# Optimization experiments

Hardware: AMD Instinct MI355X
Metric: run time of the kernel (lower is better)

## Reference

```python
import jax, jax.numpy as jnp
import numpy as np
from jax import lax

B, C, H, W = 8, 256, 128, 128
O = 256
KH, KW = 1, 3
PH, PW = 0, 1
K = KH * KW


def setup_inputs() -> dict:
    key = jax.random.key(0)
    k1, k2, k3, k4 = jax.random.split(key, 4)
    x = jax.random.normal(k1, (B, C, H, W), jnp.float32)
    # offset-predicting conv (small init so sample points stay near the grid)
    offset_w = jax.random.normal(k2, (2 * K, C, KH, KW), jnp.float32) * 0.01
    offset_b = jax.random.normal(k3, (2 * K,), jnp.float32) * 0.01
    # deformable conv weight, no bias (bias=False in the module)
    deform_w = jax.random.normal(k4, (O, C, KH, KW), jnp.float32) * (1.0 / np.sqrt(C * K))
    return {"x": x, "offset_w": offset_w, "offset_b": offset_b, "deform_w": deform_w}


def _gather_corner(x_flat, yi, xi, valid_dtype):
    # x_flat: [B, C, H*W]; yi, xi: int32 [B, K, Ho, Wo]
    valid = (yi >= 0) & (yi < H) & (xi >= 0) & (xi < W)
    yc = jnp.clip(yi, 0, H - 1)
    xc = jnp.clip(xi, 0, W - 1)
    idx = yc * W + xc  # [B, K, Ho, Wo]
    # per-batch fancy gather -> [B, C, K, Ho, Wo]
    g = jax.vmap(lambda f, i: f[:, i])(x_flat, idx)
    return g * valid[:, None].astype(valid_dtype)


def _deform_conv(x, offset, deform_w):
    # torchvision-style deform_conv2d with zero padding, groups=1, dg=1
    Ho, Wo = offset.shape[2], offset.shape[3]
    off = offset.reshape(B, K, 2, Ho, Wo)
    off_y, off_x = off[:, :, 0], off[:, :, 1]  # [B, K, Ho, Wo]

    k = jnp.arange(K)
    base_y = (-PH + (k // KW)).astype(x.dtype)[None, :, None, None]
    base_x = (-PW + (k % KW)).astype(x.dtype)[None, :, None, None]
    grid_y = jnp.arange(Ho, dtype=x.dtype)[None, None, :, None]
    grid_x = jnp.arange(Wo, dtype=x.dtype)[None, None, None, :]

    py = grid_y + base_y + off_y  # fractional sample rows [B,K,Ho,Wo]
    px = grid_x + base_x + off_x  # fractional sample cols

    y0f = jnp.floor(py)
    x0f = jnp.floor(px)
    wy = (py - y0f)[:, None]  # [B,1,K,Ho,Wo]
    wx = (px - x0f)[:, None]
    y0 = y0f.astype(jnp.int32)
    x0 = x0f.astype(jnp.int32)
    y1 = y0 + 1
    x1 = x0 + 1

    x_flat = x.reshape(B, C, H * W)
    v00 = _gather_corner(x_flat, y0, x0, x.dtype)
    v01 = _gather_corner(x_flat, y0, x1, x.dtype)
    v10 = _gather_corner(x_flat, y1, x0, x.dtype)
    v11 = _gather_corner(x_flat, y1, x1, x.dtype)

    sampled = (v00 * (1 - wy) * (1 - wx) + v01 * (1 - wy) * wx
               + v10 * wy * (1 - wx) + v11 * wy * wx)  # [B,C,K,Ho,Wo]

    return jnp.einsum('bckhw,ock->bohw', sampled, deform_w.reshape(O, C, K))


def reference(x, offset_w, offset_b, deform_w):
    # offset conv (stride 1, padding (0,1))
    offset = lax.conv_general_dilated(x, offset_w, window_strides=(1, 1),
                                      padding=[(PH, PH), (PW, PW)])
    offset = offset + offset_b[None, :, None, None]
    # in-place zeroing from the original forward
    offset = offset.at[:, 1].set(0.0).at[:, 4].set(0.0)
    return _deform_conv(x, offset, deform_w)
```

## Files before the change

kernel.cpp:

```cpp
#include <hip/hip_runtime.h>
#include <hip/hip_bf16.h>
#include <hip/hip_fp16.h>

#define Bn 8
#define Cn 256
#define Hn 128
#define Wn 128
#define On 256
#define HWn (Hn*Wn)
#define Pn  HWn
#define Rpad 896
#define W2ROW 768
#define QC  ((size_t)Pn * Cn)

typedef __attribute__((ext_vector_type(8))) short bf16x8;
typedef __attribute__((ext_vector_type(4))) float f32x4;

__device__ __forceinline__ void gload_lds16(const void* g, void* l) {
  __builtin_amdgcn_global_load_lds(
      (__attribute__((address_space(1))) void*)g,
      (__attribute__((address_space(3))) void*)l, 16, 0, 0);
}

__device__ __forceinline__ unsigned short f2bf(float f) {
  unsigned int u = __float_as_uint(f);
  unsigned int r = (u + 0x7fffu + ((u >> 16) & 1u)) >> 16;
  return (unsigned short)r;
}
__device__ __forceinline__ float bf2f(unsigned short u) {
  return __uint_as_float(((unsigned int)u) << 16);
}
__device__ __forceinline__ float h2f(unsigned int u16) {
  return __half2float(__ushort_as_half((unsigned short)u16));
}
__device__ __forceinline__ void bacc(uint4 v, float w, float* f) {
  f[0] += w * __uint_as_float(v.x << 16);
  f[1] += w * __uint_as_float(v.x & 0xffff0000u);
  f[2] += w * __uint_as_float(v.y << 16);
  f[3] += w * __uint_as_float(v.y & 0xffff0000u);
  f[4] += w * __uint_as_float(v.z << 16);
  f[5] += w * __uint_as_float(v.z & 0xffff0000u);
  f[6] += w * __uint_as_float(v.w << 16);
  f[7] += w * __uint_as_float(v.w & 0xffff0000u);
}

__global__ __launch_bounds__(256) void k_wprep(
    const float* __restrict__ dw, const float* __restrict__ ow,
    unsigned short* __restrict__ W2, unsigned short* __restrict__ Wbig) {
  int r = blockIdx.x;
  int c = threadIdx.x;
  float v = 0.f;
  if (r < 768) {
    int k = r >> 8, o = r & 255;
    v = dw[((size_t)o * Cn + c) * 3 + k];
    W2[(size_t)o * W2ROW + k * 256 + c] = f2bf(v);
  } else if (r < 786) {
    int rr = r - 768;
    int oc = rr / 3, kw = rr - 3 * oc;
    v = ow[((size_t)oc * Cn + c) * 3 + kw];
  }
  Wbig[(size_t)r * Cn + c] = f2bf(v);
}

__global__ __launch_bounds__(256) void k_transpose(
    const float* __restrict__ x, unsigned short* __restrict__ xbT) {
  int b = blockIdx.z;
  int q0 = blockIdx.x * 64, c0 = blockIdx.y * 64;
  __shared__ unsigned short t[64][66];
  int tid = threadIdx.x;
  int qq = (tid & 15) * 4;
  int cb = tid >> 4;
  const float* xb = x + (size_t)b * Cn * HWn;
  #pragma unroll
  for (int i = 0; i < 4; ++i) {
    int cl = cb + 16 * i;
    float4 v = *(const float4*)(xb + (size_t)(c0 + cl) * HWn + q0 + qq);
    unsigned lo = (unsigned)f2bf(v.x) | ((unsigned)f2bf(v.y) << 16);
    unsigned hi = (unsigned)f2bf(v.z) | ((unsigned)f2bf(v.w) << 16);
    *(unsigned*)&t[cl][qq]     = lo;
    *(unsigned*)&t[cl][qq + 2] = hi;
  }
  __syncthreads();
  unsigned short* dst = xbT + (size_t)b * QC;
  int c2 = (tid & 31) * 2, qg = tid >> 5;
  #pragma unroll
  for (int j = 0; j < 8; ++j) {
    int ql = j * 8 + qg;
    unsigned int u = (unsigned int)t[c2][ql] | ((unsigned int)t[c2 + 1][ql] << 16);
    *(unsigned int*)(dst + (size_t)(q0 + ql) * Cn + c0 + c2) = u;
  }
}

__global__ __launch_bounds__(256) void k_goff(
    const unsigned short* __restrict__ xbT,
    const unsigned short* __restrict__ Wbig,
    unsigned short* __restrict__ Goff) {
  int q0 = blockIdx.y * 128;
  const unsigned short* xb = xbT + (size_t)blockIdx.z * QC;
  unsigned short* Gz = Goff + (size_t)blockIdx.z * Pn * 32;
  __shared__ unsigned short Qs[128 * 64];
  __shared__ unsigned short Ws[128 * 64];
  int tid = threadIdx.x;
  int lane = tid & 63, wid = tid >> 6;
  int wr = wid >> 1, wc = wid & 1;
  f32x4 acc[4][4];
  #pragma unroll
  for (int m = 0; m < 4; ++m)
    #pragma unroll
    for (int n = 0; n < 4; ++n) acc[m][n] = (f32x4){0.f, 0.f, 0.f, 0.f};

  for (int kt = 0; kt < 4; ++kt) {
    int ck0 = kt * 64;
    __syncthreads();
    #pragma unroll
    for (int i = 0; i < 4; ++i) {
      int fo = wid * 1024 + i * 4096 + lane * 16;
      int row = fo >> 7;
      int slot = (fo >> 4) & 7;
      int ss = slot ^ (row & 7);
      gload_lds16(xb   + (size_t)(q0 + row) * Cn + ck0 + ss * 8, (char*)Qs + fo);
      gload_lds16(Wbig + (size_t)(768 + row) * Cn + ck0 + ss * 8, (char*)Ws + fo);
    }
    __syncthreads();
    #pragma unroll
    for (int s = 0; s < 2; ++s) {
      bf16x8 af[4], bfr[4];
      #pragma unroll
      for (int m = 0; m < 4; ++m) {
        int row = wr * 64 + m * 16 + (lane & 15);
        int slot = (s * 4 + (lane >> 4)) ^ (row & 7);
        af[m] = *(const bf16x8*)((const char*)Qs + row * 128 + slot * 16);
      }
      #pragma unroll
      for (int n = 0; n < 4; ++n) {
        int row = wc * 64 + n * 16 + (lane & 15);
        int slot = (s * 4 + (lane >> 4)) ^ (row & 7);
        bfr[n] = *(const bf16x8*)((const char*)Ws + row * 128 + slot * 16);
      }
      #pragma unroll
      for (int m = 0; m < 4; ++m)
        #pragma unroll
        for (int n = 0; n < 4; ++n)
          acc[m][n] = __builtin_amdgcn_mfma_f32_16x16x32_bf16(af[m], bfr[n], acc[m][n], 0, 0, 0);
    }
  }
  if (wc == 0) {
    #pragma unroll
    for (int m = 0; m < 4; ++m)
      #pragma unroll
      for (int n = 0; n < 2; ++n)
        #pragma unroll
        for (int rr = 0; rr < 4; ++rr) {
          int q = q0 + wr * 64 + m * 16 + (lane >> 4) * 4 + rr;
          int j = n * 16 + (lane & 15);
          if (j < 18) Gz[(size_t)q * 32 + j] = f2bf(acc[m][n][rr]);
        }
  }
}

__global__ __launch_bounds__(512) void k_fgemm(
    const unsigned short* __restrict__ xbT,
    const unsigned short* __restrict__ W2,
    const unsigned short* __restrict__ Goff,
    const float* __restrict__ obias,
    float* __restrict__ out) {
  int pt = blockIdx.x, z = blockIdx.y;
  int ho = (pt & 7) * 16 + (pt >> 3);
  const unsigned short* xz = xbT + (size_t)z * QC;
  const unsigned short* Gf = Goff + (size_t)z * Pn * 32;

  __shared__ unsigned short Qs[256 * 64];
  __shared__ unsigned short Ss[128 * 64];
  __shared__ unsigned int Sqb[128][3];
  __shared__ unsigned int Swh[128][3][2];

  int tid = threadIdx.x;
  if (tid < 384) {
    int k = tid >> 7;
    int wo = tid & 127;
    float offy = 0.f, offx = 0.f;
    int ocy = 2 * k, ocx = 2 * k + 1;
    if (ocy != 4) {
      float s = obias[ocy];
      #pragma unroll
      for (int kw = 0; kw < 3; ++kw) {
        int col = wo + kw - 1;
        if (col >= 0 && col < Wn)
          s += bf2f(Gf[(size_t)(ho * Wn + col) * 32 + ocy * 3 + kw]);
      }
      offy = s;
    }
    if (ocx != 1) {
      float s = obias[ocx];
      #pragma unroll
      for (int kw = 0; kw < 3; ++kw) {
        int col = wo + kw - 1;
        if (col >= 0 && col < Wn)
          s += bf2f(Gf[(size_t)(ho * Wn + col) * 32 + ocx * 3 + kw]);
      }
      offx = s;
    }
    float py = (float)ho + offy;
    float px = (float)(wo + k - 1) + offx;
    float y0f = floorf(py), x0f = floorf(px);
    float wy = py - y0f, wx = px - x0f;
    int y0 = (int)y0f, x0 = (int)x0f;
    int y1 = y0 + 1, x1 = x0 + 1;
    bool vy0 = (y0 >= 0) && (y0 < Hn), vy1 = (y1 >= 0) && (y1 < Hn);
    bool vx0 = (x0 >= 0) && (x0 < Wn), vx1 = (x1 >= 0) && (x1 < Wn);
    int yc0 = min(max(y0, 0), Hn - 1), yc1 = min(max(y1, 0), Hn - 1);
    int xc0 = min(max(x0, 0), Wn - 1), xc1 = min(max(x1, 0), Wn - 1);
    float w00 = (vy0 && vx0) ? (1.f - wy) * (1.f - wx) : 0.f;
    float w01 = (vy0 && vx1) ? (1.f - wy) * wx : 0.f;
    float w10 = (vy1 && vx0) ? wy * (1.f - wx) : 0.f;
    float w11 = (vy1 && vx1) ? wy * wx : 0.f;
    Sqb[wo][k] = (unsigned)yc0 | ((unsigned)xc0 << 8) | ((unsigned)yc1 << 16) | ((unsigned)xc1 << 24);
    unsigned short h00 = __half_as_ushort(__float2half_rn(w00));
    unsigned short h01 = __half_as_ushort(__float2half_rn(w01));
    unsigned short h10 = __half_as_ushort(__float2half_rn(w10));
    unsigned short h11 = __half_as_ushort(__float2half_rn(w11));
    Swh[wo][k][0] = (unsigned)h00 | ((unsigned)h01 << 16);
    Swh[wo][k][1] = (unsigned)h10 | ((unsigned)h11 << 16);
  }

  int lane = tid & 63, wid = tid >> 6;
  int lg = lane >> 4;
  int wr = wid >> 1, wc = wid & 1;
  int oct = tid & 7, pg = tid >> 3;
  int plA = pg, plB = pg + 64;
  f32x4 acc[4][4];
  #pragma unroll
  for (int m = 0; m < 4; ++m)
    #pragma unroll
    for (int n = 0; n < 4; ++n) acc[m][n] = (f32x4){0.f, 0.f, 0.f, 0.f};

  __syncthreads();

  const char* xzb = (const char*)xz;
  int octo = oct * 16;
  int dsA = plA * 128 + ((oct ^ (plA & 7)) << 4);
  int dsB = plB * 128 + ((oct ^ (plB & 7)) << 4);

  uint4 gA0, gA1, gA2, gA3, gB0, gB1, gB2, gB3;
  unsigned wpa0, wpa1, wpb0, wpb1;

  #define PREF(KT) do {                                                        \
    int kk = (KT) >> 2;                                                        \
    const char* bse = xzb + (((KT) & 3) << 7) + octo;                          \
    unsigned qpA = Sqb[plA][kk], qpB = Sqb[plB][kk];                           \
    wpa0 = Swh[plA][kk][0]; wpa1 = Swh[plA][kk][1];                            \
    wpb0 = Swh[plB][kk][0]; wpb1 = Swh[plB][kk][1];                            \
    int yA0 = (int)(qpA & 255u) << 16, xA0 = (int)((qpA >> 8) & 255u) << 9;    \
    int yA1 = (int)((qpA >> 16) & 255u) << 16, xA1 = (int)(qpA >> 24) << 9;    \
    int yB0 = (int)(qpB & 255u) << 16, xB0 = (int)((qpB >> 8) & 255u) << 9;    \
    int yB1 = (int)((qpB >> 16) & 255u) << 16, xB1 = (int)(qpB >> 24) << 9;    \
    gA0 = *(const uint4*)(bse + yA0 + xA0);                                    \
    gA1 = *(const uint4*)(bse + yA0 + xA1);                                    \
    gA2 = *(const uint4*)(bse + yA1 + xA0);                                    \
    gA3 = *(const uint4*)(bse + yA1 + xA1);                                    \
    gB0 = *(const uint4*)(bse + yB0 + xB0);                                    \
    gB1 = *(const uint4*)(bse + yB0 + xB1);                                    \
    gB2 = *(const uint4*)(bse + yB1 + xB0);                                    \
    gB3 = *(const uint4*)(bse + yB1 + xB1);                                    \
  } while (0)

  PREF(0);

  #pragma unroll
  for (int kt = 0; kt < 12; ++kt) {
    int k = kt >> 2;
    int c0 = (kt & 3) << 6;
    __syncthreads();
    #pragma unroll
    for (int i = 0; i < 4; ++i) {
      int t = tid + i * 512;
      int fo = t << 4;
      int row = fo >> 7;
      int slot = (fo >> 4) & 7;
      int ss = slot ^ (row & 7);
      gload_lds16(W2 + (size_t)row * W2ROW + k * 256 + c0 + ss * 8, (char*)Qs + fo);
    }
    {
      float f[8] = {0.f, 0.f, 0.f, 0.f, 0.f, 0.f, 0.f, 0.f};
      bacc(gA0, h2f(wpa0 & 0xffffu), f); bacc(gA1, h2f(wpa0 >> 16), f);
      bacc(gA2, h2f(wpa1 & 0xffffu), f); bacc(gA3, h2f(wpa1 >> 16), f);
      uint4 r;
      r.x = (unsigned)f2bf(f[0]) | ((unsigned)f2bf(f[1]) << 16);
      r.y = (unsigned)f2bf(f[2]) | ((unsigned)f2bf(f[3]) << 16);
      r.z = (unsigned)f2bf(f[4]) | ((unsigned)f2bf(f[5]) << 16);
      r.w = (unsigned)f2bf(f[6]) | ((unsigned)f2bf(f[7]) << 16);
      *(uint4*)((char*)Ss + dsA) = r;
    }
    {
      float f[8] = {0.f, 0.f, 0.f, 0.f, 0.f, 0.f, 0.f, 0.f};
      bacc(gB0, h2f(wpb0 & 0xffffu), f); bacc(gB1, h2f(wpb0 >> 16), f);
      bacc(gB2, h2f(wpb1 & 0xffffu), f); bacc(gB3, h2f(wpb1 >> 16), f);
      uint4 r;
      r.x = (unsigned)f2bf(f[0]) | ((unsigned)f2bf(f[1]) << 16);
      r.y = (unsigned)f2bf(f[2]) | ((unsigned)f2bf(f[3]) << 16);
      r.z = (unsigned)f2bf(f[4]) | ((unsigned)f2bf(f[5]) << 16);
      r.w = (unsigned)f2bf(f[6]) | ((unsigned)f2bf(f[7]) << 16);
      *(uint4*)((char*)Ss + dsB) = r;
    }
    __syncthreads();
    if (kt < 11) PREF(kt + 1);
    #pragma unroll
    for (int s = 0; s < 2; ++s) {
      bf16x8 af[4], bfr[4];
      #pragma unroll
      for (int m = 0; m < 4; ++m) {
        int row = wr * 64 + m * 16 + (lane & 15);
        int slot = (s * 4 + lg) ^ (row & 7);
        af[m] = *(const bf16x8*)((const char*)Qs + row * 128 + slot * 16);
      }
      #pragma unroll
      for (int n = 0; n < 4; ++n) {
        int row = wc * 64 + n * 16 + (lane & 15);
        int slot = (s * 4 + lg) ^ (row & 7);
        bfr[n] = *(const bf16x8*)((const char*)Ss + row * 128 + slot * 16);
      }
      #pragma unroll
      for (int m = 0; m < 4; ++m)
        #pragma unroll
        for (int n = 0; n < 4; ++n)
          acc[m][n] = __builtin_amdgcn_mfma_f32_16x16x32_bf16(af[m], bfr[n], acc[m][n], 0, 0, 0);
    }
  }
  #undef PREF

  float* ob_ = out + (size_t)z * On * Pn + (size_t)ho * Wn;
  #pragma unroll
  for (int m = 0; m < 4; ++m)
    #pragma unroll
    for (int n = 0; n < 4; ++n)
      #pragma unroll
      for (int rr = 0; rr < 4; ++rr) {
        int o = wr * 64 + m * 16 + lg * 4 + rr;
        int pc = wc * 64 + n * 16 + (lane & 15);
        ob_[(size_t)o * Pn + pc] = acc[m][n][rr];
      }
}

extern "C" void kernel_launch(void* const* d_in, const int* in_sizes, int n_in,
                              void* d_out, int out_size, void* d_ws, size_t ws_size,
                              hipStream_t stream) {
  const float* x  = (const float*)d_in[0];
  const float* ow = (const float*)d_in[1];
  const float* ob = (const float*)d_in[2];
  const float* dw = (const float*)d_in[3];
  float* out = (float*)d_out;

  char* ws = (char*)d_ws;
  size_t w2_bytes   = (size_t)On * W2ROW * 2;
  size_t wbig_bytes = (size_t)Rpad * Cn * 2;
  size_t xbT_bytes  = QC * 2;
  size_t w2_al   = (w2_bytes + 255) & ~(size_t)255;
  size_t wbig_al = (wbig_bytes + 255) & ~(size_t)255;

  unsigned short* W2   = (unsigned short*)ws;
  unsigned short* Wbig = (unsigned short*)(ws + w2_al);
  unsigned short* xbT  = (unsigned short*)(ws + w2_al + wbig_al);
  unsigned short* Goff = (unsigned short*)(ws + w2_al + wbig_al + (size_t)Bn * xbT_bytes);
  (void)ws_size;

  k_wprep<<<Rpad, 256, 0, stream>>>(dw, ow, W2, Wbig);
  k_transpose<<<dim3(256, 4, Bn), 256, 0, stream>>>(x, xbT);
  k_goff<<<dim3(1, 128, Bn), 256, 0, stream>>>(xbT, Wbig, Goff);
  k_fgemm<<<dim3(128, Bn), 512, 0, stream>>>(xbT, W2, Goff, ob, out);
}
```

Before: 171.0 us.

## Fuse offset-conv GEMM into main deformable GEMM kernel via LDS

Removes the separate k_goff kernel and instead computes the 18-channel offset projection for the current output row inside k_fgemm, using a small MFMA loop over the row's 128 pixels and storing the results in LDS. This avoids a kernel launch, a global write and re-read of the Goff buffer, and a second full read of xbT. Weight prep now produces a compact 32-row offset-weight matrix instead of a padded 128-row block. In exchange, each fgemm block does extra work and synchronisation up front and uses more LDS, which may lower occupancy.

```diff
diff --git a/kernel.cpp b/kernel.cpp
--- a/kernel.cpp
+++ b/kernel.cpp
@@ -9,7 +9,6 @@
 #define On 256
 #define HWn (Hn*Wn)
 #define Pn  HWn
-#define Rpad 896
 #define W2ROW 768
 #define QC  ((size_t)Pn * Cn)
 
@@ -46,20 +45,18 @@
 
 __global__ __launch_bounds__(256) void k_wprep(
     const float* __restrict__ dw, const float* __restrict__ ow,
-    unsigned short* __restrict__ W2, unsigned short* __restrict__ Wbig) {
+    unsigned short* __restrict__ W2, unsigned short* __restrict__ Woff) {
   int r = blockIdx.x;
   int c = threadIdx.x;
-  float v = 0.f;
   if (r < 768) {
     int k = r >> 8, o = r & 255;
-    v = dw[((size_t)o * Cn + c) * 3 + k];
-    W2[(size_t)o * W2ROW + k * 256 + c] = f2bf(v);
-  } else if (r < 786) {
+    W2[(size_t)o * W2ROW + k * 256 + c] = f2bf(dw[((size_t)o * Cn + c) * 3 + k]);
+  } else {
     int rr = r - 768;
-    int oc = rr / 3, kw = rr - 3 * oc;
-    v = ow[((size_t)oc * Cn + c) * 3 + kw];
-  }
-  Wbig[(size_t)r * Cn + c] = f2bf(v);
+    float v = 0.f;
+    if (rr < 18) { int oc = rr / 3, kw = rr - 3 * oc; v = ow[((size_t)oc * Cn + c) * 3 + kw]; }
+    Woff[(size_t)rr * Cn + c] = f2bf(v);
+  }
 }
 
 __global__ __launch_bounds__(256) void k_transpose(
@@ -91,90 +88,70 @@
   }
 }
 
-__global__ __launch_bounds__(256) void k_goff(
-    const unsigned short* __restrict__ xbT,
-    const unsigned short* __restrict__ Wbig,
-    unsigned short* __restrict__ Goff) {
-  int q0 = blockIdx.y * 128;
-  const unsigned short* xb = xbT + (size_t)blockIdx.z * QC;
-  unsigned short* Gz = Goff + (size_t)blockIdx.z * Pn * 32;
-  __shared__ unsigned short Qs[128 * 64];
-  __shared__ unsigned short Ws[128 * 64];
-  int tid = threadIdx.x;
-  int lane = tid & 63, wid = tid >> 6;
-  int wr = wid >> 1, wc = wid & 1;
-  f32x4 acc[4][4];
-  #pragma unroll
-  for (int m = 0; m < 4; ++m)
-    #pragma unroll
-    for (int n = 0; n < 4; ++n) acc[m][n] = (f32x4){0.f, 0.f, 0.f, 0.f};
-
-  for (int kt = 0; kt < 4; ++kt) {
-    int ck0 = kt * 64;
-    __syncthreads();
-    #pragma unroll
-    for (int i = 0; i < 4; ++i) {
-      int fo = wid * 1024 + i * 4096 + lane * 16;
-      int row = fo >> 7;
-      int slot = (fo >> 4) & 7;
-      int ss = slot ^ (row & 7);
-      gload_lds16(xb   + (size_t)(q0 + row) * Cn + ck0 + ss * 8, (char*)Qs + fo);
-      gload_lds16(Wbig + (size_t)(768 + row) * Cn + ck0 + ss * 8, (char*)Ws + fo);
-    }
-    __syncthreads();
-    #pragma unroll
-    for (int s = 0; s < 2; ++s) {
-      bf16x8 af[4], bfr[4];
-      #pragma unroll
-      for (int m = 0; m < 4; ++m) {
-        int row = wr * 64 + m * 16 + (lane & 15);
-        int slot = (s * 4 + (lane >> 4)) ^ (row & 7);
-        af[m] = *(const bf16x8*)((const char*)Qs + row * 128 + slot * 16);
-      }
-      #pragma unroll
-      for (int n = 0; n < 4; ++n) {
-        int row = wc * 64 + n * 16 + (lane & 15);
-        int slot = (s * 4 + (lane >> 4)) ^ (row & 7);
-        bfr[n] = *(const bf16x8*)((const char*)Ws + row * 128 + slot * 16);
-      }
-      #pragma unroll
-      for (int m = 0; m < 4; ++m)
-        #pragma unroll
-        for (int n = 0; n < 4; ++n)
-          acc[m][n] = __builtin_amdgcn_mfma_f32_16x16x32_bf16(af[m], bfr[n], acc[m][n], 0, 0, 0);
-    }
-  }
-  if (wc == 0) {
-    #pragma unroll
-    for (int m = 0; m < 4; ++m)
-      #pragma unroll
-      for (int n = 0; n < 2; ++n)
-        #pragma unroll
-        for (int rr = 0; rr < 4; ++rr) {
-          int q = q0 + wr * 64 + m * 16 + (lane >> 4) * 4 + rr;
-          int j = n * 16 + (lane & 15);
-          if (j < 18) Gz[(size_t)q * 32 + j] = f2bf(acc[m][n][rr]);
-        }
-  }
-}
-
 __global__ __launch_bounds__(512) void k_fgemm(
     const unsigned short* __restrict__ xbT,
     const unsigned short* __restrict__ W2,
-    const unsigned short* __restrict__ Goff,
+    const unsigned short* __restrict__ Woff,
     const float* __restrict__ obias,
     float* __restrict__ out) {
   int pt = blockIdx.x, z = blockIdx.y;
   int ho = (pt & 7) * 16 + (pt >> 3);
   const unsigned short* xz = xbT + (size_t)z * QC;
-  const unsigned short* Gf = Goff + (size_t)z * Pn * 32;
 
   __shared__ unsigned short Qs[256 * 64];
   __shared__ unsigned short Ss[128 * 64];
+  __shared__ unsigned short Goff_lds[128][32];
   __shared__ unsigned int Sqb[128][3];
   __shared__ unsigned int Swh[128][3][2];
 
   int tid = threadIdx.x;
+  int lane = tid & 63, wid = tid >> 6;
+  int lg = lane >> 4;
+  int q0p = ho * Wn;
+
+  {
+    f32x4 aco0 = (f32x4){0.f, 0.f, 0.f, 0.f};
+    f32x4 aco1 = (f32x4){0.f, 0.f, 0.f, 0.f};
+    for (int kt = 0; kt < 4; ++kt) {
+      int ck0 = kt * 64;
+      __syncthreads();
+      #pragma unroll
+      for (int i = 0; i < 2; ++i) {
+        int t = tid + i * 512;
+        int fo = t << 4;
+        int row = fo >> 7, slot = (fo >> 4) & 7, ss2 = slot ^ (row & 7);
+        gload_lds16(xz + (size_t)(q0p + row) * Cn + ck0 + ss2 * 8, (char*)Qs + fo);
+      }
+      if (tid < 256) {
+        int fo = tid << 4;
+        int row = fo >> 7, slot = (fo >> 4) & 7, ss2 = slot ^ (row & 7);
+        gload_lds16(Woff + (size_t)row * Cn + ck0 + ss2 * 8, (char*)Ss + fo);
+      }
+      __syncthreads();
+      #pragma unroll
+      for (int s = 0; s < 2; ++s) {
+        int arow = wid * 16 + (lane & 15);
+        int aslot = (s * 4 + lg) ^ (arow & 7);
+        bf16x8 af = *(const bf16x8*)((const char*)Qs + arow * 128 + aslot * 16);
+        int brow0 = (lane & 15);
+        int bslot0 = (s * 4 + lg) ^ (brow0 & 7);
+        bf16x8 bf0 = *(const bf16x8*)((const char*)Ss + brow0 * 128 + bslot0 * 16);
+        aco0 = __builtin_amdgcn_mfma_f32_16x16x32_bf16(af, bf0, aco0, 0, 0, 0);
+        int brow1 = 16 + (lane & 15);
+        int bslot1 = (s * 4 + lg) ^ (brow1 & 7);
+        bf16x8 bf1 = *(const bf16x8*)((const char*)Ss + brow1 * 128 + bslot1 * 16);
+        aco1 = __builtin_amdgcn_mfma_f32_16x16x32_bf16(af, bf1, aco1, 0, 0, 0);
+      }
+    }
+    #pragma unroll
+    for (int rr = 0; rr < 4; ++rr) {
+      int qrow = wid * 16 + lg * 4 + rr;
+      Goff_lds[qrow][(lane & 15)]      = f2bf(aco0[rr]);
+      Goff_lds[qrow][16 + (lane & 15)] = f2bf(aco1[rr]);
+    }
+  }
+  __syncthreads();
+
   if (tid < 384) {
     int k = tid >> 7;
     int wo = tid & 127;
@@ -186,7 +163,7 @@
       for (int kw = 0; kw < 3; ++kw) {
         int col = wo + kw - 1;
         if (col >= 0 && col < Wn)
-          s += bf2f(Gf[(size_t)(ho * Wn + col) * 32 + ocy * 3 + kw]);
+          s += bf2f(Goff_lds[col][ocy * 3 + kw]);
       }
       offy = s;
     }
@@ -196,7 +173,7 @@
       for (int kw = 0; kw < 3; ++kw) {
         int col = wo + kw - 1;
         if (col >= 0 && col < Wn)
-          s += bf2f(Gf[(size_t)(ho * Wn + col) * 32 + ocx * 3 + kw]);
+          s += bf2f(Goff_lds[col][ocx * 3 + kw]);
       }
       offx = s;
     }
@@ -223,8 +200,6 @@
     Swh[wo][k][1] = (unsigned)h10 | ((unsigned)h11 << 16);
   }
 
-  int lane = tid & 63, wid = tid >> 6;
-  int lg = lane >> 4;
   int wr = wid >> 1, wc = wid & 1;
   int oct = tid & 7, pg = tid >> 3;
   int plA = pg, plB = pg + 64;
@@ -352,19 +327,17 @@
 
   char* ws = (char*)d_ws;
   size_t w2_bytes   = (size_t)On * W2ROW * 2;
-  size_t wbig_bytes = (size_t)Rpad * Cn * 2;
+  size_t woff_bytes = (size_t)32 * Cn * 2;
   size_t xbT_bytes  = QC * 2;
   size_t w2_al   = (w2_bytes + 255) & ~(size_t)255;
-  size_t wbig_al = (wbig_bytes + 255) & ~(size_t)255;
+  size_t woff_al = (woff_bytes + 255) & ~(size_t)255;
 
   unsigned short* W2   = (unsigned short*)ws;
-  unsigned short* Wbig = (unsigned short*)(ws + w2_al);
-  unsigned short* xbT  = (unsigned short*)(ws + w2_al + wbig_al);
-  unsigned short* Goff = (unsigned short*)(ws + w2_al + wbig_al + (size_t)Bn * xbT_bytes);
-  (void)ws_size;
-
-  k_wprep<<<Rpad, 256, 0, stream>>>(dw, ow, W2, Wbig);
+  unsigned short* Woff = (unsigned short*)(ws + w2_al);
+  unsigned short* xbT  = (unsigned short*)(ws + w2_al + woff_al);
+  (void)ws_size; (void)xbT_bytes;
+
+  k_wprep<<<800, 256, 0, stream>>>(dw, ow, W2, Woff);
   k_transpose<<<dim3(256, 4, Bn), 256, 0, stream>>>(x, xbT);
-  k_goff<<<dim3(1, 128, Bn), 256, 0, stream>>>(xbT, Wbig, Goff);
-  k_fgemm<<<dim3(128, Bn), 512, 0, stream>>>(xbT, W2, Goff, ob, out);
-}
+  k_fgemm<<<dim3(128, Bn), 512, 0, stream>>>(xbT, W2, Woff, ob, out);
+}
```

New measurement: 169.1 us. Within noise of the previous version (-1.1%).
